# Optimization experiments

Hardware: AMD Instinct MI355X
Metric: run time of the kernel (lower is better)

## Reference

```python
import jax, jax.numpy as jnp
import numpy as np

T, B, I, H = 512, 64, 512, 512

def _glorot(key, shape):
    fan_in, fan_out = shape
    std = np.sqrt(2.0 / (fan_in + fan_out))
    return (jax.random.normal(key, shape, dtype=jnp.float32) * std)

def setup_inputs() -> dict:
    key = jax.random.key(0)
    ks = jax.random.split(key, 9)
    inp = {"X": jax.random.normal(ks[0], (T, B, I), dtype=jnp.float32)}
    names = ["Wa_x", "Wi_x", "Wf_x", "Wo_x"]
    for n, k in zip(names, ks[1:5]):
        inp[n] = _glorot(k, (I, H))
    names_h = ["Wa_h", "Wi_h", "Wf_h", "Wo_h"]
    for n, k in zip(names_h, ks[5:9]):
        inp[n] = _glorot(k, (H, H))
    for n in ["ba", "bi", "bf", "bo"]:
        inp[n] = jnp.zeros((H,), dtype=jnp.float32)
    return inp

def reference(X, Wa_x, Wi_x, Wf_x, Wo_x, Wa_h, Wi_h, Wf_h, Wo_h, ba, bi, bf, bo):
    # Precompute input projections for all timesteps: [T,B,H] each
    Xa = jnp.einsum('tbi,ih->tbh', X, Wa_x) + ba
    Xi = jnp.einsum('tbi,ih->tbh', X, Wi_x) + bi
    Xf = jnp.einsum('tbi,ih->tbh', X, Wf_x) + bf
    Xo = jnp.einsum('tbi,ih->tbh', X, Wo_x) + bo

    def step(carry, xt):
        h, s = carry
        xa, xi, xf, xo = xt
        # At t=0 h=0 and s=0, which matches the original's special-cased first step
        a = jnp.tanh(xa + h @ Wa_h)
        i = jax.nn.sigmoid(xi + h @ Wi_h)
        f = jax.nn.sigmoid(xf + h @ Wf_h)
        o = jax.nn.sigmoid(xo + h @ Wo_h)
        s_new = a * i + s * f
        h_new = jnp.tanh(s_new) * o
        return (h_new, s_new), h_new

    h0 = jnp.zeros((B, H), dtype=X.dtype)
    s0 = jnp.zeros((B, H), dtype=X.dtype)
    _, hs = jax.lax.scan(step, (h0, s0), (Xa, Xi, Xf, Xo))
    return hs  # [T, B, H] (return_sequences=True)
```

## Files before the change

### kernel.cpp

```cpp
#include <hip/hip_runtime.h>
#include <cmath>


typedef __attribute__((ext_vector_type(8)))  short   short8;
typedef __attribute__((ext_vector_type(4)))  short   short4v;
typedef __attribute__((ext_vector_type(4)))  float   f32x4;
typedef __attribute__((ext_vector_type(16))) float   f32x16;

#define TSTEPS 512

__device__ __forceinline__ unsigned short f2bf(float f) {
  unsigned u = __builtin_bit_cast(unsigned, f);
  unsigned r = (u + 0x7FFFu + ((u >> 16) & 1u)) >> 16;
  return (unsigned short)r;
}
__device__ __forceinline__ float bf2f(unsigned short s) {
  unsigned u = ((unsigned)s) << 16;
  return __builtin_bit_cast(float, u);
}
__device__ __forceinline__ void gload_lds16(const void* g, void* l) {
  __builtin_amdgcn_global_load_lds(
      (const __attribute__((address_space(1))) unsigned int*)g,
      (__attribute__((address_space(3))) unsigned int*)l, 16, 0, 0);
}
__device__ __forceinline__ float sigmoid_fast(float x) {
  return 1.0f / (1.0f + __expf(-x));
}
__device__ __forceinline__ float tanh_fast(float x) {
  float e = __expf(2.0f * x);
  return 1.0f - 2.0f / (e + 1.0f);
}

__global__ __launch_bounds__(256) void prep_wT(
    const float* __restrict__ Wax, const float* __restrict__ Wix,
    const float* __restrict__ Wfx, const float* __restrict__ Wox,
    const float* __restrict__ Wah, const float* __restrict__ Wih,
    const float* __restrict__ Wfh, const float* __restrict__ Woh,
    unsigned short* __restrict__ WxT, unsigned short* __restrict__ WhT) {
  __shared__ float tile[32][33];
  int bx = blockIdx.x;
  int mat = bx >> 8;
  int t32 = bx & 255;
  int k0 = (t32 & 15) * 32;
  int h0 = (t32 >> 4) * 32;
  const float* S =
      (mat == 0) ? Wax : (mat == 1) ? Wix : (mat == 2) ? Wfx :
      (mat == 3) ? Wox : (mat == 4) ? Wah : (mat == 5) ? Wih :
      (mat == 6) ? Wfh : Woh;
  unsigned short* D = (mat < 4) ? WxT : WhT;
  int g = mat & 3;
  int tx = threadIdx.x & 31, ty = threadIdx.x >> 5;
#pragma unroll
  for (int r = 0; r < 4; ++r)
    tile[ty + r * 8][tx] = S[(size_t)(k0 + ty + r * 8) * 512 + h0 + tx];
  __syncthreads();
#pragma unroll
  for (int r = 0; r < 4; ++r) {
    int h = h0 + ty + r * 8;
    int k = k0 + tx;
    D[((size_t)(g * 512 + h) << 9) + k] = f2bf(tile[tx][ty + r * 8]);
  }
}

__global__ __launch_bounds__(256) void prep_xbf(const float* __restrict__ X,
                                                unsigned short* __restrict__ Xbf) {
  size_t i = (size_t)blockIdx.x * 256 + threadIdx.x;
  f32x4 v = *(const f32x4*)(X + i * 4);
  short4v o;
  o[0] = (short)f2bf(v[0]); o[1] = (short)f2bf(v[1]);
  o[2] = (short)f2bf(v[2]); o[3] = (short)f2bf(v[3]);
  *(short4v*)(Xbf + i * 4) = o;
}

__global__ __launch_bounds__(256) void prep_bias(
    const float* __restrict__ ba, const float* __restrict__ bi,
    const float* __restrict__ bf, const float* __restrict__ bo,
    float* __restrict__ biascat) {
  int n = blockIdx.x * 256 + threadIdx.x;
  int g = n >> 9, h = n & 511;
  const float* s = (g == 0) ? ba : (g == 1) ? bi : (g == 2) ? bf : bo;
  biascat[n] = s[h];
}

__global__ __launch_bounds__(256) void gemm_xproj(
    const unsigned short* __restrict__ Xbf,
    const unsigned short* __restrict__ WxT,
    const float* __restrict__ biascat,
    unsigned short* __restrict__ Xg) {
  __shared__ unsigned short Asm[128 * 64];
  __shared__ unsigned short Bsm[128 * 64];
  int bx = blockIdx.x;
  int nt = bx & 15, mt = bx >> 4;
  int m0 = mt * 128, n0 = nt * 128;
  int tid = threadIdx.x;
  int w = tid >> 6, l = tid & 63;
  int wm = (w >> 1) * 64, wn = (w & 1) * 64;
  f32x4 acc[4][4] = {};

  for (int ks = 0; ks < 8; ++ks) {
    int k0 = ks * 64;
    __syncthreads();
    int lr = l >> 3;
    int ksl = ((l & 7) ^ lr) * 8;
#pragma unroll
    for (int ii = 0; ii < 4; ++ii) {
      int i = w * 4 + ii;
      int r = i * 8 + lr;
      gload_lds16(Xbf + (size_t)(m0 + r) * 512 + k0 + ksl, Asm + i * 512 + l * 8);
    }
#pragma unroll
    for (int ii = 0; ii < 4; ++ii) {
      int i = w * 4 + ii;
      int r = i * 8 + lr;
      gload_lds16(WxT + (size_t)(n0 + r) * 512 + k0 + ksl, Bsm + i * 512 + l * 8);
    }
    __syncthreads();
#pragma unroll
    for (int kk = 0; kk < 2; ++kk) {
      short8 af[4], bfr[4];
#pragma unroll
      for (int mi = 0; mi < 4; ++mi) {
        int row = wm + mi * 16 + (l & 15);
        int slot = (kk * 4 + (l >> 4)) ^ (row & 7);
        af[mi] = *(const short8*)(Asm + row * 64 + slot * 8);
      }
#pragma unroll
      for (int ni = 0; ni < 4; ++ni) {
        int row = wn + ni * 16 + (l & 15);
        int slot = (kk * 4 + (l >> 4)) ^ (row & 7);
        bfr[ni] = *(const short8*)(Bsm + row * 64 + slot * 8);
      }
#pragma unroll
      for (int mi = 0; mi < 4; ++mi)
#pragma unroll
        for (int ni = 0; ni < 4; ++ni)
          acc[mi][ni] = __builtin_amdgcn_mfma_f32_16x16x32_bf16(
              af[mi], bfr[ni], acc[mi][ni], 0, 0, 0);
    }
  }
#pragma unroll
  for (int mi = 0; mi < 4; ++mi)
#pragma unroll
    for (int ni = 0; ni < 4; ++ni) {
      int col = n0 + wn + ni * 16 + (l & 15);
      float bias = biascat[col];
      int g = col >> 9, h = col & 511;
      int chunk = h >> 3, e = h & 7;
#pragma unroll
      for (int r = 0; r < 4; ++r) {
        int m = m0 + wm + mi * 16 + (l >> 4) * 4 + r;
        int t = m >> 6, b = m & 63;
        Xg[(((size_t)(t * 4 + g) * 64 + chunk) * 64 + b) * 8 + e] =
            f2bf(acc[mi][ni][r] + bias);
      }
    }
}

__global__ __launch_bounds__(256, 1) void lstm_scan(
    const unsigned short* __restrict__ Xg,
    const unsigned short* __restrict__ WhT,
    unsigned short* __restrict__ hbuf,
    int* __restrict__ flags,
    float* __restrict__ out) {
  __shared__ unsigned short hsm[2][64 * 32 * 8];
  const int j = blockIdx.x;
  const int mi = j & 1;
  const int cc = j >> 1;
  const int tid = threadIdx.x;
  const int w = tid >> 6, l = tid & 63;

  short8 wf[32];
  {
    const int m = l & 31;
    const int g = m >> 3;
    const int hcol_w = cc * 32 + w * 8 + (m & 7);
    const unsigned short* base =
        WhT + (((size_t)(g * 512 + hcol_w)) << 9) + (l >> 5) * 8;
#pragma unroll
    for (int kt = 0; kt < 32; ++kt) wf[kt] = *(const short8*)(base + kt * 16);
  }

  const int b = mi * 32 + (l & 31);
  const int hcol0 = cc * 32 + w * 8 + (l >> 5) * 4;
  const int mychunk = cc * 4 + w;

  const unsigned stg_goff0 = (unsigned)((l >> 5) * 1024 + (mi * 32 + (l & 31)) * 16);
  const int stg_loff0 = w * 8192 + l * 16;
  const int ld_loff0 = (l >> 5) * 512 + (l & 31) * 16;
  const unsigned st_voff = (unsigned)(mychunk * 1024 + b * 16 + (l >> 5) * 8);

  int* const myflag = flags + (mi * 16 + cc) * 32;
  int* const pollflag = flags + (mi * 16 + (l & 15)) * 32;

  float s4[4] = {0.f, 0.f, 0.f, 0.f};

  uint2 xgn[4];
#pragma unroll
  for (int g = 0; g < 4; ++g)
    xgn[g] = *(const uint2*)(Xg +
        ((((size_t)(0 * 4 + g) * 64 + mychunk) * 64 + b) * 8 + (l >> 5) * 4));

#pragma unroll 1
  for (int t = 0; t < TSTEPS; ++t) {
    f32x16 asum = {};
    if (t > 0) {
      int fv;
      do {
        fv = __hip_atomic_load(pollflag, __ATOMIC_RELAXED,
                               __HIP_MEMORY_SCOPE_AGENT);
      } while (!__all(fv >= t));
      asm volatile("" ::: "memory");
      const unsigned short* hbase = hbuf + (size_t)((t - 1) & 1) * 32768;
      unsigned short* hs = hsm[(t - 1) & 1];
      short8 tmp[8];
#pragma unroll
      for (int i = 0; i < 8; ++i) {
        asm volatile("global_load_dwordx4 %0, %1, %2 sc0 sc1"
                     : "=v"(tmp[i])
                     : "v"(stg_goff0 + (unsigned)((w * 8 + i) * 2048)),
                       "s"(hbase));
      }
      asm volatile("s_waitcnt vmcnt(0)" ::: "memory");
      __builtin_amdgcn_sched_barrier(0);
#pragma unroll
      for (int i = 0; i < 8; ++i)
        *(short8*)((char*)hs + stg_loff0 + i * 1024) = tmp[i];
      __syncthreads();
      f32x16 a0 = {}, a1 = {};
#pragma unroll
      for (int kt = 0; kt < 32; kt += 2) {
        short8 b0 = *(const short8*)((const char*)hs + ld_loff0 + kt * 1024);
        short8 b1 = *(const short8*)((const char*)hs + ld_loff0 + (kt + 1) * 1024);
        a0 = __builtin_amdgcn_mfma_f32_32x32x16_bf16(wf[kt], b0, a0, 0, 0, 0);
        a1 = __builtin_amdgcn_mfma_f32_32x32x16_bf16(wf[kt + 1], b1, a1,
                                                     0, 0, 0);
      }
      asum = a0 + a1;
    }
    float hout[4];
#pragma unroll
    for (int q = 0; q < 4; ++q) {
      float pa = asum[0 * 4 + q] + bf2f((unsigned short)((q < 2 ? xgn[0].x : xgn[0].y) >> ((q & 1) * 16)));
      float pi = asum[1 * 4 + q] + bf2f((unsigned short)((q < 2 ? xgn[1].x : xgn[1].y) >> ((q & 1) * 16)));
      float pf = asum[2 * 4 + q] + bf2f((unsigned short)((q < 2 ? xgn[2].x : xgn[2].y) >> ((q & 1) * 16)));
      float po = asum[3 * 4 + q] + bf2f((unsigned short)((q < 2 ? xgn[3].x : xgn[3].y) >> ((q & 1) * 16)));
      float a  = tanh_fast(pa);
      float ig = sigmoid_fast(pi);
      float fg = sigmoid_fast(pf);
      float og = sigmoid_fast(po);
      s4[q] = a * ig + s4[q] * fg;
      hout[q] = tanh_fast(s4[q]) * og;
    }
    {
      unsigned lo = (unsigned)f2bf(hout[0]) | ((unsigned)f2bf(hout[1]) << 16);
      unsigned hi = (unsigned)f2bf(hout[2]) | ((unsigned)f2bf(hout[3]) << 16);
      uint2 hd; hd.x = lo; hd.y = hi;
      const unsigned short* sbase = hbuf + (size_t)(t & 1) * 32768;
      asm volatile("global_store_dwordx2 %0, %1, %2 sc0 sc1"
                   :: "v"(st_voff), "v"(hd), "s"(sbase) : "memory");
      asm volatile("s_waitcnt vmcnt(0)" ::: "memory");
      __syncthreads();
      if (tid == 0)
        __hip_atomic_store(myflag, t + 1, __ATOMIC_RELAXED,
                           __HIP_MEMORY_SCOPE_AGENT);
    }
    f32x4 ov;
    ov[0] = hout[0]; ov[1] = hout[1]; ov[2] = hout[2]; ov[3] = hout[3];
    *(f32x4*)(out + ((size_t)t * 64 + b) * 512 + hcol0) = ov;
    const int tn = (t + 1 < TSTEPS) ? t + 1 : t;
#pragma unroll
    for (int g = 0; g < 4; ++g)
      xgn[g] = *(const uint2*)(Xg +
          ((((size_t)(tn * 4 + g) * 64 + mychunk) * 64 + b) * 8 + (l >> 5) * 4));
  }
}

extern "C" void kernel_launch(void* const* d_in, const int* in_sizes, int n_in,
                              void* d_out, int out_size, void* d_ws,
                              size_t ws_size, hipStream_t stream) {
  const float* X   = (const float*)d_in[0];
  const float* Wax = (const float*)d_in[1];
  const float* Wix = (const float*)d_in[2];
  const float* Wfx = (const float*)d_in[3];
  const float* Wox = (const float*)d_in[4];
  const float* Wah = (const float*)d_in[5];
  const float* Wih = (const float*)d_in[6];
  const float* Wfh = (const float*)d_in[7];
  const float* Woh = (const float*)d_in[8];
  const float* ba  = (const float*)d_in[9];
  const float* bi  = (const float*)d_in[10];
  const float* bf  = (const float*)d_in[11];
  const float* bo  = (const float*)d_in[12];

  char* ws = (char*)d_ws;
  unsigned short* Xg   = (unsigned short*)(ws);
  unsigned short* Xbf  = (unsigned short*)(ws + 134217728);
  unsigned short* hbuf = (unsigned short*)(ws + 134217728);
  unsigned short* WxT  = (unsigned short*)(ws + 167772160);
  unsigned short* WhT  = (unsigned short*)(ws + 169869312);
  float*          bcat = (float*)(ws + 171966464);
  int*            flags= (int*)(ws + 171974656);

  hipMemsetAsync(ws + 171974656, 0, 4096, stream);

  prep_wT<<<2048, 256, 0, stream>>>(Wax, Wix, Wfx, Wox, Wah, Wih, Wfh, Woh,
                                    WxT, WhT);
  prep_xbf<<<16384, 256, 0, stream>>>(X, Xbf);
  prep_bias<<<8, 256, 0, stream>>>(ba, bi, bf, bo, bcat);
  gemm_xproj<<<4096, 256, 0, stream>>>(Xbf, WxT, bcat, Xg);
  lstm_scan<<<32, 256, 0, stream>>>(Xg, WhT, hbuf, flags, (float*)d_out);
}
```

Measured before the change: 1.764 ms.

## Fuse input-projection GEMM with LSTM scan using producer blocks and per-tile counters

```diff
diff --git a/kernel.cpp b/kernel.cpp
--- a/kernel.cpp
+++ b/kernel.cpp
@@ -82,92 +82,106 @@
   biascat[n] = s[h];
 }
 
-__global__ __launch_bounds__(256) void gemm_xproj(
+__global__ __launch_bounds__(256, 1) void lstm_fused(
     const unsigned short* __restrict__ Xbf,
     const unsigned short* __restrict__ WxT,
-    const float* __restrict__ biascat,
-    unsigned short* __restrict__ Xg) {
-  __shared__ unsigned short Asm[128 * 64];
-  __shared__ unsigned short Bsm[128 * 64];
-  int bx = blockIdx.x;
-  int nt = bx & 15, mt = bx >> 4;
-  int m0 = mt * 128, n0 = nt * 128;
-  int tid = threadIdx.x;
-  int w = tid >> 6, l = tid & 63;
-  int wm = (w >> 1) * 64, wn = (w & 1) * 64;
-  f32x4 acc[4][4] = {};
-
-  for (int ks = 0; ks < 8; ++ks) {
-    int k0 = ks * 64;
-    __syncthreads();
-    int lr = l >> 3;
-    int ksl = ((l & 7) ^ lr) * 8;
-#pragma unroll
-    for (int ii = 0; ii < 4; ++ii) {
-      int i = w * 4 + ii;
-      int r = i * 8 + lr;
-      gload_lds16(Xbf + (size_t)(m0 + r) * 512 + k0 + ksl, Asm + i * 512 + l * 8);
-    }
-#pragma unroll
-    for (int ii = 0; ii < 4; ++ii) {
-      int i = w * 4 + ii;
-      int r = i * 8 + lr;
-      gload_lds16(WxT + (size_t)(n0 + r) * 512 + k0 + ksl, Bsm + i * 512 + l * 8);
-    }
-    __syncthreads();
-#pragma unroll
-    for (int kk = 0; kk < 2; ++kk) {
-      short8 af[4], bfr[4];
-#pragma unroll
-      for (int mi = 0; mi < 4; ++mi) {
-        int row = wm + mi * 16 + (l & 15);
-        int slot = (kk * 4 + (l >> 4)) ^ (row & 7);
-        af[mi] = *(const short8*)(Asm + row * 64 + slot * 8);
-      }
-#pragma unroll
-      for (int ni = 0; ni < 4; ++ni) {
-        int row = wn + ni * 16 + (l & 15);
-        int slot = (kk * 4 + (l >> 4)) ^ (row & 7);
-        bfr[ni] = *(const short8*)(Bsm + row * 64 + slot * 8);
-      }
-#pragma unroll
-      for (int mi = 0; mi < 4; ++mi)
-#pragma unroll
-        for (int ni = 0; ni < 4; ++ni)
-          acc[mi][ni] = __builtin_amdgcn_mfma_f32_16x16x32_bf16(
-              af[mi], bfr[ni], acc[mi][ni], 0, 0, 0);
-    }
-  }
-#pragma unroll
-  for (int mi = 0; mi < 4; ++mi)
-#pragma unroll
-    for (int ni = 0; ni < 4; ++ni) {
-      int col = n0 + wn + ni * 16 + (l & 15);
-      float bias = biascat[col];
-      int g = col >> 9, h = col & 511;
-      int chunk = h >> 3, e = h & 7;
-#pragma unroll
-      for (int r = 0; r < 4; ++r) {
-        int m = m0 + wm + mi * 16 + (l >> 4) * 4 + r;
-        int t = m >> 6, b = m & 63;
-        Xg[(((size_t)(t * 4 + g) * 64 + chunk) * 64 + b) * 8 + e] =
-            f2bf(acc[mi][ni][r] + bias);
-      }
-    }
-}
-
-__global__ __launch_bounds__(256, 1) void lstm_scan(
-    const unsigned short* __restrict__ Xg,
+    const float* __restrict__ bcat,
+    unsigned short* __restrict__ Xg,
     const unsigned short* __restrict__ WhT,
     unsigned short* __restrict__ hbuf,
     int* __restrict__ flags,
+    int* __restrict__ xcnt,
     float* __restrict__ out) {
-  __shared__ unsigned short hsm[2][64 * 32 * 8];
+  __shared__ unsigned short smem[32768];
+  const int tid = threadIdx.x;
+  const int w = tid >> 6, l = tid & 63;
+
+  if (blockIdx.x >= 32) {
+    unsigned short* Asm_ = smem;
+    unsigned short* Bsm_ = smem + 8192;
+    const int wkr = blockIdx.x - 32;
+    const int wm = (w >> 1) * 64, wn = (w & 1) * 64;
+#pragma unroll 1
+    for (int id = wkr; id < 4096; id += 512) {
+      const int mt = id >> 4, nt = id & 15;
+      const int m0 = mt * 128, n0 = nt * 128;
+      f32x4 acc[4][4] = {};
+      for (int ks = 0; ks < 8; ++ks) {
+        int k0 = ks * 64;
+        __syncthreads();
+        int lr = l >> 3;
+        int ksl = ((l & 7) ^ lr) * 8;
+#pragma unroll
+        for (int ii = 0; ii < 4; ++ii) {
+          int i = w * 4 + ii;
+          int r = i * 8 + lr;
+          gload_lds16(Xbf + (size_t)(m0 + r) * 512 + k0 + ksl,
+                      Asm_ + i * 512 + l * 8);
+        }
+#pragma unroll
+        for (int ii = 0; ii < 4; ++ii) {
+          int i = w * 4 + ii;
+          int r = i * 8 + lr;
+          gload_lds16(WxT + (size_t)(n0 + r) * 512 + k0 + ksl,
+                      Bsm_ + i * 512 + l * 8);
+        }
+        __syncthreads();
+#pragma unroll
+        for (int kk = 0; kk < 2; ++kk) {
+          short8 af[4], bfr[4];
+#pragma unroll
+          for (int mi = 0; mi < 4; ++mi) {
+            int row = wm + mi * 16 + (l & 15);
+            int slot = (kk * 4 + (l >> 4)) ^ (row & 7);
+            af[mi] = *(const short8*)(Asm_ + row * 64 + slot * 8);
+          }
+#pragma unroll
+          for (int ni = 0; ni < 4; ++ni) {
+            int row = wn + ni * 16 + (l & 15);
+            int slot = (kk * 4 + (l >> 4)) ^ (row & 7);
+            bfr[ni] = *(const short8*)(Bsm_ + row * 64 + slot * 8);
+          }
+#pragma unroll
+          for (int mi = 0; mi < 4; ++mi)
+#pragma unroll
+            for (int ni = 0; ni < 4; ++ni)
+              acc[mi][ni] = __builtin_amdgcn_mfma_f32_16x16x32_bf16(
+                  af[mi], bfr[ni], acc[mi][ni], 0, 0, 0);
+        }
+      }
+#pragma unroll
+      for (int mi = 0; mi < 4; ++mi)
+#pragma unroll
+        for (int ni = 0; ni < 4; ++ni) {
+          int col = n0 + wn + ni * 16 + (l & 15);
+          float bias = bcat[col];
+          int g = col >> 9, h = col & 511;
+          int chunk = h >> 3, e = h & 7;
+#pragma unroll
+          for (int r = 0; r < 4; ++r) {
+            int m = m0 + wm + mi * 16 + (l >> 4) * 4 + r;
+            int tt = m >> 6, bb = m & 63;
+            unsigned off =
+                (unsigned)(((((tt * 4 + g) * 64 + chunk) * 64 + bb) * 8 + e) * 2);
+            unsigned val = (unsigned)f2bf(acc[mi][ni][r] + bias);
+            asm volatile("global_store_short %0, %1, %2 sc0 sc1"
+                         :: "v"(off), "v"(val), "s"(Xg) : "memory");
+          }
+        }
+      asm volatile("s_waitcnt vmcnt(0)" ::: "memory");
+      __syncthreads();
+      if (tid == 0)
+        __hip_atomic_fetch_add(xcnt + mt, 1, __ATOMIC_RELAXED,
+                               __HIP_MEMORY_SCOPE_AGENT);
+    }
+    return;
+  }
+
+  unsigned short* hsm0 = smem;
+  unsigned short* hsm1 = smem + 16384;
   const int j = blockIdx.x;
   const int mi = j & 1;
   const int cc = j >> 1;
-  const int tid = threadIdx.x;
-  const int w = tid >> 6, l = tid & 63;
 
   short8 wf[32];
   {
@@ -181,13 +195,15 @@
   }
 
   const int b = mi * 32 + (l & 31);
-  const int hcol0 = cc * 32 + w * 8 + (l >> 5) * 4;
+  const int half = l >> 5;
+  const int hcol0 = cc * 32 + w * 8 + half * 4;
   const int mychunk = cc * 4 + w;
 
-  const unsigned stg_goff0 = (unsigned)((l >> 5) * 1024 + (mi * 32 + (l & 31)) * 16);
+  const unsigned stg_goff0 = (unsigned)(half * 1024 + (mi * 32 + (l & 31)) * 16);
   const int stg_loff0 = w * 8192 + l * 16;
-  const int ld_loff0 = (l >> 5) * 512 + (l & 31) * 16;
-  const unsigned st_voff = (unsigned)(mychunk * 1024 + b * 16 + (l >> 5) * 8);
+  const int ld_loff0 = half * 512 + (l & 31) * 16;
+  const unsigned st_voff = (unsigned)(mychunk * 1024 + b * 16 + half * 8);
+  const unsigned xg_lane_off = (unsigned)(((mychunk * 64 + b) * 8 + half * 4) * 2);
 
   int* const myflag = flags + (mi * 16 + cc) * 32;
   int* const pollflag = flags + (mi * 16 + (l & 15)) * 32;
@@ -195,23 +211,39 @@
   float s4[4] = {0.f, 0.f, 0.f, 0.f};
 
   uint2 xgn[4];
-#pragma unroll
-  for (int g = 0; g < 4; ++g)
-    xgn[g] = *(const uint2*)(Xg +
-        ((((size_t)(0 * 4 + g) * 64 + mychunk) * 64 + b) * 8 + (l >> 5) * 4));
+  {
+    int cv;
+    do {
+      cv = __hip_atomic_load(xcnt, __ATOMIC_RELAXED, __HIP_MEMORY_SCOPE_AGENT);
+    } while (!__all(cv >= 16));
+    asm volatile("" ::: "memory");
+#pragma unroll
+    for (int g = 0; g < 4; ++g) {
+      unsigned off = (unsigned)((0 * 4 + g) * 64 * 64 * 8 * 2) + xg_lane_off;
+      asm volatile("global_load_dwordx2 %0, %1, %2 sc0 sc1"
+                   : "=v"(xgn[g]) : "v"(off), "s"(Xg));
+    }
+    asm volatile("s_waitcnt vmcnt(0)" ::: "memory");
+    __builtin_amdgcn_sched_barrier(0);
+  }
 
 #pragma unroll 1
   for (int t = 0; t < TSTEPS; ++t) {
     f32x16 asum = {};
+    uint2 xgn_nx[4];
+    const int tn = (t + 1 < TSTEPS) ? t + 1 : TSTEPS - 1;
     if (t > 0) {
-      int fv;
+      const int mtn = tn >> 1;
+      int fv, cv;
       do {
         fv = __hip_atomic_load(pollflag, __ATOMIC_RELAXED,
                                __HIP_MEMORY_SCOPE_AGENT);
-      } while (!__all(fv >= t));
+        cv = __hip_atomic_load(xcnt + mtn, __ATOMIC_RELAXED,
+                               __HIP_MEMORY_SCOPE_AGENT);
+      } while (!__all((fv >= t) && (cv >= 16)));
       asm volatile("" ::: "memory");
       const unsigned short* hbase = hbuf + (size_t)((t - 1) & 1) * 32768;
-      unsigned short* hs = hsm[(t - 1) & 1];
+      unsigned short* hs = ((t - 1) & 1) ? hsm1 : hsm0;
       short8 tmp[8];
 #pragma unroll
       for (int i = 0; i < 8; ++i) {
@@ -219,6 +251,12 @@
                      : "=v"(tmp[i])
                      : "v"(stg_goff0 + (unsigned)((w * 8 + i) * 2048)),
                        "s"(hbase));
+      }
+#pragma unroll
+      for (int g = 0; g < 4; ++g) {
+        unsigned off = (unsigned)((tn * 4 + g) * 64 * 64 * 8 * 2) + xg_lane_off;
+        asm volatile("global_load_dwordx2 %0, %1, %2 sc0 sc1"
+                     : "=v"(xgn_nx[g]) : "v"(off), "s"(Xg));
       }
       asm volatile("s_waitcnt vmcnt(0)" ::: "memory");
       __builtin_amdgcn_sched_barrier(0);
@@ -236,6 +274,15 @@
                                                      0, 0, 0);
       }
       asum = a0 + a1;
+    } else {
+#pragma unroll
+      for (int g = 0; g < 4; ++g) {
+        unsigned off = (unsigned)((tn * 4 + g) * 64 * 64 * 8 * 2) + xg_lane_off;
+        asm volatile("global_load_dwordx2 %0, %1, %2 sc0 sc1"
+                     : "=v"(xgn_nx[g]) : "v"(off), "s"(Xg));
+      }
+      asm volatile("s_waitcnt vmcnt(0)" ::: "memory");
+      __builtin_amdgcn_sched_barrier(0);
     }
     float hout[4];
 #pragma unroll
@@ -267,11 +314,8 @@
     f32x4 ov;
     ov[0] = hout[0]; ov[1] = hout[1]; ov[2] = hout[2]; ov[3] = hout[3];
     *(f32x4*)(out + ((size_t)t * 64 + b) * 512 + hcol0) = ov;
-    const int tn = (t + 1 < TSTEPS) ? t + 1 : t;
-#pragma unroll
-    for (int g = 0; g < 4; ++g)
-      xgn[g] = *(const uint2*)(Xg +
-          ((((size_t)(tn * 4 + g) * 64 + mychunk) * 64 + b) * 8 + (l >> 5) * 4));
+#pragma unroll
+    for (int g = 0; g < 4; ++g) xgn[g] = xgn_nx[g];
   }
 }
 
@@ -295,18 +339,19 @@
   char* ws = (char*)d_ws;
   unsigned short* Xg   = (unsigned short*)(ws);
   unsigned short* Xbf  = (unsigned short*)(ws + 134217728);
-  unsigned short* hbuf = (unsigned short*)(ws + 134217728);
   unsigned short* WxT  = (unsigned short*)(ws + 167772160);
   unsigned short* WhT  = (unsigned short*)(ws + 169869312);
   float*          bcat = (float*)(ws + 171966464);
   int*            flags= (int*)(ws + 171974656);
-
-  hipMemsetAsync(ws + 171974656, 0, 4096, stream);
+  int*            xcnt = (int*)(ws + 171978752);
+  unsigned short* hbuf = (unsigned short*)(ws + 171980800);
+
+  hipMemsetAsync(ws + 171974656, 0, 4096 + 1024, stream);
 
   prep_wT<<<2048, 256, 0, stream>>>(Wax, Wix, Wfx, Wox, Wah, Wih, Wfh, Woh,
                                     WxT, WhT);
   prep_xbf<<<16384, 256, 0, stream>>>(X, Xbf);
   prep_bias<<<8, 256, 0, stream>>>(ba, bi, bf, bo, bcat);
-  gemm_xproj<<<4096, 256, 0, stream>>>(Xbf, WxT, bcat, Xg);
-  lstm_scan<<<32, 256, 0, stream>>>(Xg, WhT, hbuf, flags, (float*)d_out);
-}
+  lstm_fused<<<544, 256, 0, stream>>>(Xbf, WxT, bcat, Xg, WhT, hbuf, flags,
+                                      xcnt, (float*)d_out);
+}
```

After: 1.889 ms. +7.1%, slower.
